# Performance work log

Hardware: AMD Instinct MI355X
Metric: run time of the kernel (lower is better)

## Reference

```python
import jax, jax.numpy as jnp
import numpy as np

B, T, IN, EMB, HID, L, OUT = 64, 1024, 512, 512, 512, 4, 512


def setup_inputs() -> dict:
    key = jax.random.key(0)
    ks = jax.random.split(key, 12)
    s = 0.05  # small init scale to keep gates well-conditioned
    return {
        "x": jax.random.normal(ks[0], (B, T, IN), jnp.float32),
        # input projection (torch Linear: weight [out, in])
        "w_in": jax.random.normal(ks[1], (EMB, IN), jnp.float32) * s,
        "b_in": jnp.zeros((EMB,), jnp.float32),
        # stacked GRU weights (layer input size == EMB == HID for all layers)
        # gate order matches torch: [reset, update, new], each block HID rows
        "w_ih": jax.random.normal(ks[2], (L, 3 * HID, EMB), jnp.float32) * s,
        "w_hh": jax.random.normal(ks[3], (L, 3 * HID, HID), jnp.float32) * s,
        "b_ih": jnp.zeros((L, 3 * HID), jnp.float32),
        "b_hh": jnp.zeros((L, 3 * HID), jnp.float32),
        # output MLP: Linear(HID->EMB), ReLU, Linear(EMB->OUT)
        "w_o1": jax.random.normal(ks[4], (EMB, HID), jnp.float32) * s,
        "b_o1": jnp.zeros((EMB,), jnp.float32),
        "w_o2": jax.random.normal(ks[5], (OUT, EMB), jnp.float32) * s,
        "b_o2": jnp.zeros((OUT,), jnp.float32),
    }


def _gru_layer(xs, wih, whh, bih, bhh):
    """One GRU layer, batch_first input xs: [B, T, E] -> [B, T, H].
    PyTorch GRU math:
      r = sig(Wir x + bir + Whr h + bhr)
      z = sig(Wiz x + biz + Whz h + bhz)
      n = tanh(Win x + bin + r * (Whn h + bhn))
      h' = (1 - z) * n + z * h
    """
    # Precompute all input-side gate projections in one big GEMM: [B, T, 3H]
    gi = jnp.einsum('bte,ge->btg', xs, wih) + bih
    gi = jnp.swapaxes(gi, 0, 1)  # [T, B, 3H] for scan over time
    h0 = jnp.zeros((xs.shape[0], whh.shape[1]), xs.dtype)

    def step(h, gi_t):
        gh = h @ whh.T + bhh  # [B, 3H]
        i_r, i_z, i_n = jnp.split(gi_t, 3, axis=-1)
        h_r, h_z, h_n = jnp.split(gh, 3, axis=-1)
        r = jax.nn.sigmoid(i_r + h_r)
        z = jax.nn.sigmoid(i_z + h_z)
        n = jnp.tanh(i_n + r * h_n)
        h_new = (1.0 - z) * n + z * h
        return h_new, h_new

    _, ys = jax.lax.scan(step, h0, gi)  # ys: [T, B, H]
    return jnp.swapaxes(ys, 0, 1)


def reference(x, w_in, b_in, w_ih, w_hh, b_ih, b_hh, w_o1, b_o1, w_o2, b_o2):
    # input Linear + ReLU
    h = jax.nn.relu(x @ w_in.T + b_in)  # [B, T, EMB]
    # stacked GRU (num_layers fixed, structurally distinct weights)
    for l in range(L):
        h = _gru_layer(h, w_ih[l], w_hh[l], b_ih[l], b_hh[l])
    # output MLP: Linear -> ReLU -> Linear
    out = jax.nn.relu(h @ w_o1.T + b_o1) @ w_o2.T + b_o2  # [B, T, OUT]
    return out
```

## Files before the change

### kernel.cpp

```cpp
#include <hip/hip_runtime.h>
#include <hip/hip_bf16.h>

typedef __attribute__((ext_vector_type(8))) __bf16 bf16x8;
typedef __attribute__((ext_vector_type(4))) float f32x4;
typedef __attribute__((ext_vector_type(4))) int i32x4;

constexpr int B_N = 64;
constexpr int T_N = 1024;
constexpr int H_N = 512;
constexpr long long BT_N = (long long)B_N * T_N;

__global__ void cvt_f32_bf16(const float* __restrict__ src,
                             __hip_bfloat16* __restrict__ dst, long long n4)
{
    long long i = (long long)blockIdx.x * blockDim.x + threadIdx.x;
    long long stride = (long long)gridDim.x * blockDim.x;
    for (; i < n4; i += stride) {
        float4 v = ((const float4*)src)[i];
        __hip_bfloat16* d = dst + i * 4;
        d[0] = __float2bfloat16(v.x);
        d[1] = __float2bfloat16(v.y);
        d[2] = __float2bfloat16(v.z);
        d[3] = __float2bfloat16(v.w);
    }
}

__device__ inline void store_val(float* p, float v) { *p = v; }
__device__ inline void store_val(__hip_bfloat16* p, float v) { *p = __float2bfloat16(v); }

template <typename OutT, bool RELU>
__global__ __launch_bounds__(256)
void mfma_gemm(const __hip_bfloat16* __restrict__ A,
               const __hip_bfloat16* __restrict__ W,
               const float* __restrict__ bias,
               OutT* __restrict__ C, int M, int N, int K)
{
    constexpr int LDT = 72;
    __shared__ __hip_bfloat16 Asl[128 * LDT];
    __shared__ __hip_bfloat16 Bsl[128 * LDT];

    const int tid  = threadIdx.x;
    const int wv   = tid >> 6;
    const int lane = tid & 63;
    const int quad = lane >> 4;
    const int l16  = lane & 15;
    const int bm = blockIdx.y, bn = blockIdx.x;
    const int m0w = (wv & 1) * 64;
    const int n0w = (wv >> 1) * 64;

    f32x4 acc[4][4] = {};

    for (int k0 = 0; k0 < K; k0 += 64) {
        __syncthreads();
#pragma unroll
        for (int i = 0; i < 4; ++i) {
            int c = tid + i * 256;
            int row = c >> 3, ch = c & 7;
            bf16x8 va = *(const bf16x8*)(A + (size_t)(bm * 128 + row) * K + k0 + ch * 8);
            bf16x8 vb = *(const bf16x8*)(W + (size_t)(bn * 128 + row) * K + k0 + ch * 8);
            *(bf16x8*)(Asl + row * LDT + ch * 8) = va;
            *(bf16x8*)(Bsl + row * LDT + ch * 8) = vb;
        }
        __syncthreads();
#pragma unroll
        for (int kc = 0; kc < 2; ++kc) {
            const int koff = kc * 32 + quad * 8;
            bf16x8 af[4], bfr[4];
#pragma unroll
            for (int mt = 0; mt < 4; ++mt)
                af[mt] = *(const bf16x8*)(Asl + (m0w + mt * 16 + l16) * LDT + koff);
#pragma unroll
            for (int nt = 0; nt < 4; ++nt)
                bfr[nt] = *(const bf16x8*)(Bsl + (n0w + nt * 16 + l16) * LDT + koff);
#pragma unroll
            for (int mt = 0; mt < 4; ++mt)
#pragma unroll
                for (int nt = 0; nt < 4; ++nt)
                    acc[mt][nt] = __builtin_amdgcn_mfma_f32_16x16x32_bf16(
                        af[mt], bfr[nt], acc[mt][nt], 0, 0, 0);
        }
    }

#pragma unroll
    for (int nt = 0; nt < 4; ++nt) {
        const int col = bn * 128 + n0w + nt * 16 + l16;
        const float bv = bias[col];
#pragma unroll
        for (int mt = 0; mt < 4; ++mt) {
#pragma unroll
            for (int rg = 0; rg < 4; ++rg) {
                const int row = bm * 128 + m0w + mt * 16 + quad * 4 + rg;
                float v = acc[mt][nt][rg] + bv;
                if (RELU) v = fmaxf(v, 0.f);
                store_val(C + (size_t)row * N + col, v);
            }
        }
    }
}

__device__ inline float u2f(unsigned u) { union { unsigned u; float f; } c; c.u = u; return c.f; }
__device__ inline float sigm(float x) { return 1.f / (1.f + __expf(-x)); }

__global__ __launch_bounds__(384)
void gru_scan_grp(const __hip_bfloat16* __restrict__ gi,
                  const __hip_bfloat16* __restrict__ whh,
                  const float* __restrict__ bhh,
                  __hip_bfloat16* __restrict__ y,
                  unsigned* __restrict__ bar)
{
    constexpr int LROW = 1040;
    __shared__ __align__(16) char hsl[16 * LROW];
    __shared__ float ghl[3][16][66];

    const int tid  = threadIdx.x;
    const int wv   = tid >> 6;
    const int lane = tid & 63;
    const int quad = lane >> 4;
    const int l16  = lane & 15;
    const int grp  = blockIdx.x >> 3;
    const int slc  = blockIdx.x & 7;
    const int j0   = slc * 64;
    const int m0   = grp * 16;
    const int g    = wv >> 1;
    const int jt   = wv & 1;
    unsigned* cnt = bar + grp * 1024;

    const int colg = g * 512 + j0 + jt * 32;
    bf16x8 bfrag[2][16];
#pragma unroll
    for (int nt = 0; nt < 2; ++nt)
#pragma unroll
        for (int kc = 0; kc < 16; ++kc)
            bfrag[nt][kc] = *(const bf16x8*)(whh + (size_t)(colg + nt * 16 + l16) * 512
                                             + kc * 32 + quad * 8);

    for (int c = tid; c < 16 * LROW / 16; c += 384)
        ((i32x4*)hsl)[c] = (i32x4)0;

    const int um = tid >> 5;
    const int jp = tid & 31;
    float br0 = 0, br1 = 0, bz0 = 0, bz1 = 0, bn0 = 0, bn1 = 0;
    const __hip_bfloat16* gip[2] = {nullptr, nullptr};
    __hip_bfloat16* ysp[2] = {nullptr, nullptr};
    int hof[2] = {0, 0};
    if (tid < 256) {
        const int jg = j0 + 2 * jp;
        br0 = bhh[jg];         br1 = bhh[jg + 1];
        bz0 = bhh[512 + jg];   bz1 = bhh[512 + jg + 1];
        bn0 = bhh[1024 + jg];  bn1 = bhh[1024 + jg + 1];
#pragma unroll
        for (int p = 0; p < 2; ++p) {
            const int mg = m0 + p * 8 + um;
            gip[p] = gi + (size_t)mg * 1024 * 1536 + jg;
            ysp[p] = y  + (size_t)mg * 1024 * 512  + jg;
            hof[p] = (p * 8 + um) * LROW + jg * 2;
        }
    }

    const int mr  = tid >> 6;
    const int bof = (tid & 63) * 16;
    const char* yre[4] = {nullptr, nullptr, nullptr, nullptr};
    int dst[4] = {0, 0, 0, 0};
    if (tid < 256) {
#pragma unroll
        for (int q = 0; q < 4; ++q) {
            const int m = mr + q * 4;
            yre[q] = (const char*)(y + (size_t)(m0 + m) * 1024 * 512) + bof;
            dst[q] = m * LROW + bof;
        }
    }

    const int abase = l16 * LROW + quad * 16;

    __syncthreads();

#pragma unroll 1
    for (int t = 0; t < 1024; ++t) {
        unsigned pr[2], pz[2], pn[2];
        if (tid < 256) {
#pragma unroll
            for (int p = 0; p < 2; ++p) {
                pr[p] = *(const unsigned*)(gip[p]);
                pz[p] = *(const unsigned*)(gip[p] + 512);
                pn[p] = *(const unsigned*)(gip[p] + 1024);
                gip[p] += 1536;
            }
        }

        f32x4 a0 = {}, a1 = {};
        if (t > 0) {
#pragma unroll
            for (int kc = 0; kc < 16; ++kc) {
                bf16x8 af = *(const bf16x8*)(hsl + abase + kc * 64);
                a0 = __builtin_amdgcn_mfma_f32_16x16x32_bf16(af, bfrag[0][kc], a0, 0, 0, 0);
                a1 = __builtin_amdgcn_mfma_f32_16x16x32_bf16(af, bfrag[1][kc], a1, 0, 0, 0);
            }
        }
#pragma unroll
        for (int rg = 0; rg < 4; ++rg) {
            ghl[g][quad * 4 + rg][jt * 32 + l16]      = a0[rg];
            ghl[g][quad * 4 + rg][jt * 32 + 16 + l16] = a1[rg];
        }
        __syncthreads();

        if (tid < 256) {
#pragma unroll
            for (int p = 0; p < 2; ++p) {
                const int m = p * 8 + um;
                const float2 gr = *(const float2*)&ghl[0][m][jp * 2];
                const float2 gz = *(const float2*)&ghl[1][m][jp * 2];
                const float2 gn = *(const float2*)&ghl[2][m][jp * 2];
                const unsigned hpk = *(const unsigned*)(hsl + hof[p]);
                const float hp0 = u2f(hpk << 16), hp1 = u2f(hpk & 0xffff0000u);
                const float r0 = sigm(u2f(pr[p] << 16)         + gr.x + br0);
                const float r1 = sigm(u2f(pr[p] & 0xffff0000u) + gr.y + br1);
                const float z0 = sigm(u2f(pz[p] << 16)         + gz.x + bz0);
                const float z1 = sigm(u2f(pz[p] & 0xffff0000u) + gz.y + bz1);
                const float n0 = tanhf(u2f(pn[p] << 16)         + r0 * (gn.x + bn0));
                const float n1 = tanhf(u2f(pn[p] & 0xffff0000u) + r1 * (gn.y + bn1));
                const float h0 = (1.f - z0) * n0 + z0 * hp0;
                const float h1 = (1.f - z1) * n1 + z1 * hp1;
                const unsigned outv =
                    (unsigned)__bfloat16_as_ushort(__float2bfloat16(h0)) |
                    ((unsigned)__bfloat16_as_ushort(__float2bfloat16(h1)) << 16);
                asm volatile("global_store_dword %0, %1, off sc0 sc1"
                             :: "v"((void*)ysp[p]), "v"(outv) : "memory");
                ysp[p] += 512;
            }
        }
        __syncthreads();

        if (tid == 0) {
            __hip_atomic_fetch_add(&cnt[t], 1u, __ATOMIC_RELAXED, __HIP_MEMORY_SCOPE_AGENT);
            while (__hip_atomic_load(&cnt[t], __ATOMIC_RELAXED, __HIP_MEMORY_SCOPE_AGENT) < 8u)
                __builtin_amdgcn_s_sleep(2);
        }
        __syncthreads();

        if (t < 1023) {
            if (tid < 256) {
                i32x4 v0, v1, v2, v3;
                asm volatile(
                    "global_load_dwordx4 %0, %4, off sc0 sc1\n\t"
                    "global_load_dwordx4 %1, %5, off sc0 sc1\n\t"
                    "global_load_dwordx4 %2, %6, off sc0 sc1\n\t"
                    "global_load_dwordx4 %3, %7, off sc0 sc1\n\t"
                    "s_waitcnt vmcnt(0)"
                    : "=&v"(v0), "=&v"(v1), "=&v"(v2), "=&v"(v3)
                    : "v"((const void*)yre[0]), "v"((const void*)yre[1]),
                      "v"((const void*)yre[2]), "v"((const void*)yre[3])
                    : "memory");
                *(i32x4*)(hsl + dst[0]) = v0;
                *(i32x4*)(hsl + dst[1]) = v1;
                *(i32x4*)(hsl + dst[2]) = v2;
                *(i32x4*)(hsl + dst[3]) = v3;
                yre[0] += 1024; yre[1] += 1024; yre[2] += 1024; yre[3] += 1024;
            }
            __syncthreads();
        }
    }
}

extern "C" void kernel_launch(void* const* d_in, const int* in_sizes, int n_in,
                              void* d_out, int out_size, void* d_ws, size_t ws_size,
                              hipStream_t stream)
{
    const float* x    = (const float*)d_in[0];
    const float* w_in = (const float*)d_in[1];
    const float* b_in = (const float*)d_in[2];
    const float* w_ih = (const float*)d_in[3];
    const float* w_hh = (const float*)d_in[4];
    const float* b_ih = (const float*)d_in[5];
    const float* b_hh = (const float*)d_in[6];
    const float* w_o1 = (const float*)d_in[7];
    const float* b_o1 = (const float*)d_in[8];
    const float* w_o2 = (const float*)d_in[9];
    const float* b_o2 = (const float*)d_in[10];
    float* out = (float*)d_out;

    char* ws = (char*)d_ws;
    const size_t GI_BYTES  = (size_t)BT_N * 1536 * 2;
    const size_t ACT_BYTES = (size_t)BT_N * 512 * 2;
    const size_t WT_BYTES  = (size_t)7077888 * 2;
    __hip_bfloat16* gi   = (__hip_bfloat16*)ws;
    __hip_bfloat16* act  = (__hip_bfloat16*)(ws + GI_BYTES);
    __hip_bfloat16* wbf  = (__hip_bfloat16*)(ws + GI_BYTES + ACT_BYTES);
    unsigned*       bar  = (unsigned*)(ws + GI_BYTES + ACT_BYTES + WT_BYTES);
    __hip_bfloat16* xbf  = gi;
    __hip_bfloat16* tmp  = gi;

    __hip_bfloat16* w_in_bf = wbf;
    __hip_bfloat16* w_ih_bf = wbf + 262144;
    __hip_bfloat16* w_hh_bf = w_ih_bf + 3145728;
    __hip_bfloat16* w_o1_bf = w_hh_bf + 3145728;
    __hip_bfloat16* w_o2_bf = w_o1_bf + 262144;

    hipMemsetAsync(bar, 0, (size_t)4 * 4 * 1024 * sizeof(unsigned), stream);

    cvt_f32_bf16<<<256, 256, 0, stream>>>(w_in, w_in_bf, 262144 / 4);
    cvt_f32_bf16<<<1024, 256, 0, stream>>>(w_ih, w_ih_bf, 3145728 / 4);
    cvt_f32_bf16<<<1024, 256, 0, stream>>>(w_hh, w_hh_bf, 3145728 / 4);
    cvt_f32_bf16<<<256, 256, 0, stream>>>(w_o1, w_o1_bf, 262144 / 4);
    cvt_f32_bf16<<<256, 256, 0, stream>>>(w_o2, w_o2_bf, 262144 / 4);
    cvt_f32_bf16<<<4096, 256, 0, stream>>>(x, xbf, BT_N * 512 / 4);

    const int M = (int)BT_N;

    mfma_gemm<__hip_bfloat16, true><<<dim3(4, 512), 256, 0, stream>>>(
        xbf, w_in_bf, b_in, act, M, 512, 512);

    for (int l = 0; l < 4; ++l) {
        const __hip_bfloat16* wih_l = w_ih_bf + (size_t)l * 1536 * 512;
        const __hip_bfloat16* whh_l = w_hh_bf + (size_t)l * 1536 * 512;
        const float* bih_l = b_ih + (size_t)l * 1536;
        const float* bhh_l = b_hh + (size_t)l * 1536;

        mfma_gemm<__hip_bfloat16, false><<<dim3(12, 512), 256, 0, stream>>>(
            act, wih_l, bih_l, gi, M, 1536, 512);

        gru_scan_grp<<<dim3(32), dim3(384), 0, stream>>>(
            gi, whh_l, bhh_l, act, bar + (size_t)l * 4096);
    }

    mfma_gemm<__hip_bfloat16, true><<<dim3(4, 512), 256, 0, stream>>>(
        act, w_o1_bf, b_o1, tmp, M, 512, 512);
    mfma_gemm<float, false><<<dim3(4, 512), 256, 0, stream>>>(
        tmp, w_o2_bf, b_o2, out, M, 512, 512);
}
```

Before: 13.12 ms.

## Fuse input projection into GRU scan and wavefront-pipeline all four layers

Replaces the per-layer input GEMM plus scan kernel pair with one persistent kernel of 256 blocks covering all four layers. Each block keeps both W_ih and W_hh slices in registers and computes the input-side gate projection per timestep alongside the recurrent one. Layer l waits on layer l-1's per-timestep counters, so layers run as a time-skewed pipeline. This removes the large gi round-trip through global memory and overlaps the four layers' serial scans. The cost is more MFMA work per step, an extra global load of x each step, a waitcnt after every store, and the need for all 256 blocks to be co-resident for the spin barriers.

```diff
diff --git a/kernel.cpp b/kernel.cpp
--- a/kernel.cpp
+++ b/kernel.cpp
@@ -7,7 +7,6 @@
 
 constexpr int B_N = 64;
 constexpr int T_N = 1024;
-constexpr int H_N = 512;
 constexpr long long BT_N = (long long)B_N * T_N;
 
 __global__ void cvt_f32_bf16(const float* __restrict__ src,
@@ -100,161 +99,202 @@
 
 __device__ inline float u2f(unsigned u) { union { unsigned u; float f; } c; c.u = u; return c.f; }
 __device__ inline float sigm(float x) { return 1.f / (1.f + __expf(-x)); }
+__device__ inline void spin_ge(unsigned* p, unsigned v)
+{
+    while (__hip_atomic_load(p, __ATOMIC_ACQUIRE, __HIP_MEMORY_SCOPE_AGENT) < v)
+        __builtin_amdgcn_s_sleep(2);
+}
 
 __global__ __launch_bounds__(384)
-void gru_scan_grp(const __hip_bfloat16* __restrict__ gi,
-                  const __hip_bfloat16* __restrict__ whh,
-                  const float* __restrict__ bhh,
-                  __hip_bfloat16* __restrict__ y,
-                  unsigned* __restrict__ bar)
+void gru_fused(__hip_bfloat16* __restrict__ act,
+               __hip_bfloat16* __restrict__ ybuf,
+               const __hip_bfloat16* __restrict__ wihb,
+               const __hip_bfloat16* __restrict__ whhb,
+               const float* __restrict__ bihf,
+               const float* __restrict__ bhhf,
+               unsigned* __restrict__ bar)
 {
     constexpr int LROW = 1040;
+    constexpr size_t YELL = (size_t)64 * 1024 * 512;
+
     __shared__ __align__(16) char hsl[16 * LROW];
-    __shared__ float ghl[3][16][66];
+    __shared__ __align__(16) char xsl[16 * LROW];
+    __shared__ float ghl[4][16][35];
 
     const int tid  = threadIdx.x;
     const int wv   = tid >> 6;
     const int lane = tid & 63;
     const int quad = lane >> 4;
     const int l16  = lane & 15;
-    const int grp  = blockIdx.x >> 3;
-    const int slc  = blockIdx.x & 7;
-    const int j0   = slc * 64;
-    const int m0   = grp * 16;
-    const int g    = wv >> 1;
-    const int jt   = wv & 1;
-    unsigned* cnt = bar + grp * 1024;
-
-    const int colg = g * 512 + j0 + jt * 32;
-    bf16x8 bfrag[2][16];
-#pragma unroll
-    for (int nt = 0; nt < 2; ++nt)
-#pragma unroll
-        for (int kc = 0; kc < 16; ++kc)
-            bfrag[nt][kc] = *(const bf16x8*)(whh + (size_t)(colg + nt * 16 + l16) * 512
-                                             + kc * 32 + quad * 8);
+    const int layer = blockIdx.x >> 6;
+    const int grp   = (blockIdx.x >> 4) & 3;
+    const int slc   = blockIdx.x & 15;
+    const int j0 = slc * 32;
+    const int m0 = grp * 16;
+    const int g  = wv >> 1;
+    const int jt = wv & 1;
+
+    const __hip_bfloat16* in_l = (layer == 0) ? act : ybuf + (size_t)(layer - 1) * YELL;
+    __hip_bfloat16* out_l = (layer == 3) ? act : ybuf + (size_t)layer * YELL;
+    const __hip_bfloat16* wih_l = wihb + (size_t)layer * 1536 * 512;
+    const __hip_bfloat16* whh_l = whhb + (size_t)layer * 1536 * 512;
+    const float* bih_l = bihf + layer * 1536;
+    const float* bhh_l = bhhf + layer * 1536;
+    unsigned* own = bar + (layer * 4 + grp) * 1024;
+    unsigned* prv = (layer > 0) ? bar + ((layer - 1) * 4 + grp) * 1024 : bar;
+
+    const int colg = g * 512 + j0 + jt * 16;
+    bf16x8 bX[16], bH[16];
+#pragma unroll
+    for (int kc = 0; kc < 16; ++kc) {
+        bX[kc] = *(const bf16x8*)(wih_l + (size_t)(colg + l16) * 512 + kc * 32 + quad * 8);
+        bH[kc] = *(const bf16x8*)(whh_l + (size_t)(colg + l16) * 512 + kc * 32 + quad * 8);
+    }
 
     for (int c = tid; c < 16 * LROW / 16; c += 384)
         ((i32x4*)hsl)[c] = (i32x4)0;
 
-    const int um = tid >> 5;
-    const int jp = tid & 31;
-    float br0 = 0, br1 = 0, bz0 = 0, bz1 = 0, bn0 = 0, bn1 = 0;
-    const __hip_bfloat16* gip[2] = {nullptr, nullptr};
-    __hip_bfloat16* ysp[2] = {nullptr, nullptr};
-    int hof[2] = {0, 0};
+    const int row = tid >> 4;
+    const int jp  = tid & 15;
+    const int jg  = j0 + 2 * jp;
+    float brA = 0, brB = 0, bzA = 0, bzB = 0, biA = 0, biB = 0, bhA = 0, bhB = 0;
+    __hip_bfloat16* ysp = nullptr;
+    int hofc = 0;
     if (tid < 256) {
-        const int jg = j0 + 2 * jp;
-        br0 = bhh[jg];         br1 = bhh[jg + 1];
-        bz0 = bhh[512 + jg];   bz1 = bhh[512 + jg + 1];
-        bn0 = bhh[1024 + jg];  bn1 = bhh[1024 + jg + 1];
-#pragma unroll
-        for (int p = 0; p < 2; ++p) {
-            const int mg = m0 + p * 8 + um;
-            gip[p] = gi + (size_t)mg * 1024 * 1536 + jg;
-            ysp[p] = y  + (size_t)mg * 1024 * 512  + jg;
-            hof[p] = (p * 8 + um) * LROW + jg * 2;
-        }
+        brA = bih_l[jg]        + bhh_l[jg];
+        brB = bih_l[jg + 1]    + bhh_l[jg + 1];
+        bzA = bih_l[512 + jg]     + bhh_l[512 + jg];
+        bzB = bih_l[512 + jg + 1] + bhh_l[512 + jg + 1];
+        biA = bih_l[1024 + jg];     biB = bih_l[1024 + jg + 1];
+        bhA = bhh_l[1024 + jg];     bhB = bhh_l[1024 + jg + 1];
+        ysp  = out_l + (size_t)(m0 + row) * 1024 * 512 + jg;
+        hofc = row * LROW + jg * 2;
     }
 
     const int mr  = tid >> 6;
     const int bof = (tid & 63) * 16;
-    const char* yre[4] = {nullptr, nullptr, nullptr, nullptr};
-    int dst[4] = {0, 0, 0, 0};
+    const char* hre[4];
+    const char* xre[4];
+    int dst[4];
     if (tid < 256) {
 #pragma unroll
         for (int q = 0; q < 4; ++q) {
             const int m = mr + q * 4;
-            yre[q] = (const char*)(y + (size_t)(m0 + m) * 1024 * 512) + bof;
+            hre[q] = (const char*)out_l + (size_t)(m0 + m) * 1048576 + bof;
+            xre[q] = (const char*)in_l  + (size_t)(m0 + m) * 1048576 + bof;
             dst[q] = m * LROW + bof;
         }
     }
 
     const int abase = l16 * LROW + quad * 16;
 
+    if (layer > 0 && tid == 0) spin_ge(prv, 16u);
+    __syncthreads();
+    if (tid < 256) {
+        i32x4 v0, v1, v2, v3;
+        asm volatile(
+            "global_load_dwordx4 %0, %4, off sc0 sc1\n\t"
+            "global_load_dwordx4 %1, %5, off sc0 sc1\n\t"
+            "global_load_dwordx4 %2, %6, off sc0 sc1\n\t"
+            "global_load_dwordx4 %3, %7, off sc0 sc1\n\t"
+            "s_waitcnt vmcnt(0)"
+            : "=&v"(v0), "=&v"(v1), "=&v"(v2), "=&v"(v3)
+            : "v"((const void*)xre[0]), "v"((const void*)xre[1]),
+              "v"((const void*)xre[2]), "v"((const void*)xre[3])
+            : "memory");
+        *(i32x4*)(xsl + dst[0]) = v0;
+        *(i32x4*)(xsl + dst[1]) = v1;
+        *(i32x4*)(xsl + dst[2]) = v2;
+        *(i32x4*)(xsl + dst[3]) = v3;
+        xre[0] += 1024; xre[1] += 1024; xre[2] += 1024; xre[3] += 1024;
+    }
     __syncthreads();
 
 #pragma unroll 1
     for (int t = 0; t < 1024; ++t) {
-        unsigned pr[2], pz[2], pn[2];
+        f32x4 aX = {}, aH = {};
+#pragma unroll
+        for (int kc = 0; kc < 16; ++kc) {
+            bf16x8 ax = *(const bf16x8*)(xsl + abase + kc * 64);
+            bf16x8 ah = *(const bf16x8*)(hsl + abase + kc * 64);
+            aX = __builtin_amdgcn_mfma_f32_16x16x32_bf16(ax, bX[kc], aX, 0, 0, 0);
+            aH = __builtin_amdgcn_mfma_f32_16x16x32_bf16(ah, bH[kc], aH, 0, 0, 0);
+        }
+        if (g < 2) {
+#pragma unroll
+            for (int rg = 0; rg < 4; ++rg)
+                ghl[g][quad * 4 + rg][jt * 16 + l16] = aX[rg] + aH[rg];
+        } else {
+#pragma unroll
+            for (int rg = 0; rg < 4; ++rg) {
+                ghl[2][quad * 4 + rg][jt * 16 + l16] = aX[rg];
+                ghl[3][quad * 4 + rg][jt * 16 + l16] = aH[rg];
+            }
+        }
+        __syncthreads();
+
         if (tid < 256) {
-#pragma unroll
-            for (int p = 0; p < 2; ++p) {
-                pr[p] = *(const unsigned*)(gip[p]);
-                pz[p] = *(const unsigned*)(gip[p] + 512);
-                pn[p] = *(const unsigned*)(gip[p] + 1024);
-                gip[p] += 1536;
+            const float sr0 = ghl[0][row][2 * jp], sr1 = ghl[0][row][2 * jp + 1];
+            const float sz0 = ghl[1][row][2 * jp], sz1 = ghl[1][row][2 * jp + 1];
+            const float si0 = ghl[2][row][2 * jp], si1 = ghl[2][row][2 * jp + 1];
+            const float sh0 = ghl[3][row][2 * jp], sh1 = ghl[3][row][2 * jp + 1];
+            const unsigned hpk = *(const unsigned*)(hsl + hofc);
+            const float hp0 = u2f(hpk << 16), hp1 = u2f(hpk & 0xffff0000u);
+            const float r0 = sigm(sr0 + brA), r1 = sigm(sr1 + brB);
+            const float z0 = sigm(sz0 + bzA), z1 = sigm(sz1 + bzB);
+            const float n0 = tanhf(si0 + biA + r0 * (sh0 + bhA));
+            const float n1 = tanhf(si1 + biB + r1 * (sh1 + bhB));
+            const float h0 = (1.f - z0) * n0 + z0 * hp0;
+            const float h1 = (1.f - z1) * n1 + z1 * hp1;
+            const unsigned outv =
+                (unsigned)__bfloat16_as_ushort(__float2bfloat16(h0)) |
+                ((unsigned)__bfloat16_as_ushort(__float2bfloat16(h1)) << 16);
+            asm volatile("global_store_dword %0, %1, off sc0 sc1\n\t"
+                         "s_waitcnt vmcnt(0)"
+                         :: "v"((void*)ysp), "v"(outv) : "memory");
+            ysp += 512;
+        }
+        __syncthreads();
+
+        if (tid == 0) {
+            __hip_atomic_fetch_add(&own[t], 1u, __ATOMIC_RELEASE, __HIP_MEMORY_SCOPE_AGENT);
+            if (t < 1023) {
+                spin_ge(&own[t], 16u);
+                if (layer > 0) spin_ge(&prv[t + 1], 16u);
             }
-        }
-
-        f32x4 a0 = {}, a1 = {};
-        if (t > 0) {
-#pragma unroll
-            for (int kc = 0; kc < 16; ++kc) {
-                bf16x8 af = *(const bf16x8*)(hsl + abase + kc * 64);
-                a0 = __builtin_amdgcn_mfma_f32_16x16x32_bf16(af, bfrag[0][kc], a0, 0, 0, 0);
-                a1 = __builtin_amdgcn_mfma_f32_16x16x32_bf16(af, bfrag[1][kc], a1, 0, 0, 0);
-            }
-        }
-#pragma unroll
-        for (int rg = 0; rg < 4; ++rg) {
-            ghl[g][quad * 4 + rg][jt * 32 + l16]      = a0[rg];
-            ghl[g][quad * 4 + rg][jt * 32 + 16 + l16] = a1[rg];
-        }
-        __syncthreads();
-
-        if (tid < 256) {
-#pragma unroll
-            for (int p = 0; p < 2; ++p) {
-                const int m = p * 8 + um;
-                const float2 gr = *(const float2*)&ghl[0][m][jp * 2];
-                const float2 gz = *(const float2*)&ghl[1][m][jp * 2];
-                const float2 gn = *(const float2*)&ghl[2][m][jp * 2];
-                const unsigned hpk = *(const unsigned*)(hsl + hof[p]);
-                const float hp0 = u2f(hpk << 16), hp1 = u2f(hpk & 0xffff0000u);
-                const float r0 = sigm(u2f(pr[p] << 16)         + gr.x + br0);
-                const float r1 = sigm(u2f(pr[p] & 0xffff0000u) + gr.y + br1);
-                const float z0 = sigm(u2f(pz[p] << 16)         + gz.x + bz0);
-                const float z1 = sigm(u2f(pz[p] & 0xffff0000u) + gz.y + bz1);
-                const float n0 = tanhf(u2f(pn[p] << 16)         + r0 * (gn.x + bn0));
-                const float n1 = tanhf(u2f(pn[p] & 0xffff0000u) + r1 * (gn.y + bn1));
-                const float h0 = (1.f - z0) * n0 + z0 * hp0;
-                const float h1 = (1.f - z1) * n1 + z1 * hp1;
-                const unsigned outv =
-                    (unsigned)__bfloat16_as_ushort(__float2bfloat16(h0)) |
-                    ((unsigned)__bfloat16_as_ushort(__float2bfloat16(h1)) << 16);
-                asm volatile("global_store_dword %0, %1, off sc0 sc1"
-                             :: "v"((void*)ysp[p]), "v"(outv) : "memory");
-                ysp[p] += 512;
-            }
-        }
-        __syncthreads();
-
-        if (tid == 0) {
-            __hip_atomic_fetch_add(&cnt[t], 1u, __ATOMIC_RELAXED, __HIP_MEMORY_SCOPE_AGENT);
-            while (__hip_atomic_load(&cnt[t], __ATOMIC_RELAXED, __HIP_MEMORY_SCOPE_AGENT) < 8u)
-                __builtin_amdgcn_s_sleep(2);
         }
         __syncthreads();
 
         if (t < 1023) {
             if (tid < 256) {
-                i32x4 v0, v1, v2, v3;
+                i32x4 h0, h1, h2, h3, x0, x1, x2, x3;
                 asm volatile(
-                    "global_load_dwordx4 %0, %4, off sc0 sc1\n\t"
-                    "global_load_dwordx4 %1, %5, off sc0 sc1\n\t"
-                    "global_load_dwordx4 %2, %6, off sc0 sc1\n\t"
-                    "global_load_dwordx4 %3, %7, off sc0 sc1\n\t"
+                    "global_load_dwordx4 %0, %8, off sc0 sc1\n\t"
+                    "global_load_dwordx4 %1, %9, off sc0 sc1\n\t"
+                    "global_load_dwordx4 %2, %10, off sc0 sc1\n\t"
+                    "global_load_dwordx4 %3, %11, off sc0 sc1\n\t"
+                    "global_load_dwordx4 %4, %12, off sc0 sc1\n\t"
+                    "global_load_dwordx4 %5, %13, off sc0 sc1\n\t"
+                    "global_load_dwordx4 %6, %14, off sc0 sc1\n\t"
+                    "global_load_dwordx4 %7, %15, off sc0 sc1\n\t"
                     "s_waitcnt vmcnt(0)"
-                    : "=&v"(v0), "=&v"(v1), "=&v"(v2), "=&v"(v3)
-                    : "v"((const void*)yre[0]), "v"((const void*)yre[1]),
-                      "v"((const void*)yre[2]), "v"((const void*)yre[3])
+                    : "=&v"(h0), "=&v"(h1), "=&v"(h2), "=&v"(h3),
+                      "=&v"(x0), "=&v"(x1), "=&v"(x2), "=&v"(x3)
+                    : "v"((const void*)hre[0]), "v"((const void*)hre[1]),
+                      "v"((const void*)hre[2]), "v"((const void*)hre[3]),
+                      "v"((const void*)xre[0]), "v"((const void*)xre[1]),
+                      "v"((const void*)xre[2]), "v"((const void*)xre[3])
                     : "memory");
-                *(i32x4*)(hsl + dst[0]) = v0;
-                *(i32x4*)(hsl + dst[1]) = v1;
-                *(i32x4*)(hsl + dst[2]) = v2;
-                *(i32x4*)(hsl + dst[3]) = v3;
-                yre[0] += 1024; yre[1] += 1024; yre[2] += 1024; yre[3] += 1024;
+                *(i32x4*)(hsl + dst[0]) = h0;
+                *(i32x4*)(hsl + dst[1]) = h1;
+                *(i32x4*)(hsl + dst[2]) = h2;
+                *(i32x4*)(hsl + dst[3]) = h3;
+                *(i32x4*)(xsl + dst[0]) = x0;
+                *(i32x4*)(xsl + dst[1]) = x1;
+                *(i32x4*)(xsl + dst[2]) = x2;
+                *(i32x4*)(xsl + dst[3]) = x3;
+                hre[0] += 1024; hre[1] += 1024; hre[2] += 1024; hre[3] += 1024;
+                xre[0] += 1024; xre[1] += 1024; xre[2] += 1024; xre[3] += 1024;
             }
             __syncthreads();
         }
@@ -279,15 +319,15 @@
     float* out = (float*)d_out;
 
     char* ws = (char*)d_ws;
-    const size_t GI_BYTES  = (size_t)BT_N * 1536 * 2;
-    const size_t ACT_BYTES = (size_t)BT_N * 512 * 2;
+    const size_t YB_BYTES  = (size_t)BT_N * 512 * 2;
+    const size_t GI_BYTES  = 3 * YB_BYTES;
     const size_t WT_BYTES  = (size_t)7077888 * 2;
-    __hip_bfloat16* gi   = (__hip_bfloat16*)ws;
+    __hip_bfloat16* ybuf = (__hip_bfloat16*)ws;
     __hip_bfloat16* act  = (__hip_bfloat16*)(ws + GI_BYTES);
-    __hip_bfloat16* wbf  = (__hip_bfloat16*)(ws + GI_BYTES + ACT_BYTES);
-    unsigned*       bar  = (unsigned*)(ws + GI_BYTES + ACT_BYTES + WT_BYTES);
-    __hip_bfloat16* xbf  = gi;
-    __hip_bfloat16* tmp  = gi;
+    __hip_bfloat16* wbf  = (__hip_bfloat16*)(ws + GI_BYTES + YB_BYTES);
+    unsigned*       bar  = (unsigned*)(ws + GI_BYTES + YB_BYTES + WT_BYTES);
+    __hip_bfloat16* xbf  = ybuf;
+    __hip_bfloat16* tmp  = ybuf;
 
     __hip_bfloat16* w_in_bf = wbf;
     __hip_bfloat16* w_ih_bf = wbf + 262144;
@@ -309,18 +349,8 @@
     mfma_gemm<__hip_bfloat16, true><<<dim3(4, 512), 256, 0, stream>>>(
         xbf, w_in_bf, b_in, act, M, 512, 512);
 
-    for (int l = 0; l < 4; ++l) {
-        const __hip_bfloat16* wih_l = w_ih_bf + (size_t)l * 1536 * 512;
-        const __hip_bfloat16* whh_l = w_hh_bf + (size_t)l * 1536 * 512;
-        const float* bih_l = b_ih + (size_t)l * 1536;
-        const float* bhh_l = b_hh + (size_t)l * 1536;
-
-        mfma_gemm<__hip_bfloat16, false><<<dim3(12, 512), 256, 0, stream>>>(
-            act, wih_l, bih_l, gi, M, 1536, 512);
-
-        gru_scan_grp<<<dim3(32), dim3(384), 0, stream>>>(
-            gi, whh_l, bhh_l, act, bar + (size_t)l * 4096);
-    }
+    gru_fused<<<dim3(256), dim3(384), 0, stream>>>(
+        act, ybuf, w_ih_bf, w_hh_bf, b_ih, b_hh, bar);
 
     mfma_gemm<__hip_bfloat16, true><<<dim3(4, 512), 256, 0, stream>>>(
         act, w_o1_bf, b_o1, tmp, M, 512, 512);
```

Result: faster. 11.67 ms (-11.1%).
